# Performance work log

Measured on AMD Instinct MI355X. Metric: run time of the kernel, lower is better.

The kernel has to match this reference:

```python
import jax, jax.numpy as jnp
import numpy as np

COMMITMENT_W = 0.1
PROXIMITY_W = 0.33

def setup_inputs() -> dict:
    key = jax.random.key(0)
    k1, k2, k3 = jax.random.split(key, 3)
    N, B, C, H, W = 2, 16, 64, 64, 64
    P, D = 16, 64
    input_data = jax.random.normal(k1, (N, B, C, H, W), dtype=jnp.float32)
    codebook = jax.random.uniform(k2, (P, D), dtype=jnp.float32, minval=-1.0 / P, maxval=1.0 / P)
    previous_active_vectors = jax.random.uniform(k3, (P, D), dtype=jnp.float32, minval=-1.0 / P, maxval=1.0 / P)
    return {"input_data": input_data, "codebook": codebook,
            "previous_active_vectors": previous_active_vectors,
            "num_active_vectors": 16}


def reference(input_data, codebook, previous_active_vectors, num_active_vectors):
    # input_data: (N, B, C, H, W); codebook: (P, D) with D == C
    D = codebook.shape[1]
    N, B, C, H, W = input_data.shape
    # (N*B, H, W, C) channels-last, matching permute(0,2,3,1)
    x = input_data.reshape(N * B, C, H, W).transpose(0, 2, 3, 1)
    flat = x.reshape(-1, D)                              # (T, D)
    x2 = jnp.sum(flat * flat, axis=1, keepdims=True)     # (T, 1)

    n_levels = int(np.log2(num_active_vectors))
    quantized_list, losses = [], []
    for level in range(n_levels):
        nv = 2 ** (level + 1)
        active = codebook[:nv]                           # (nv, D)
        # squared euclidean distances (T, nv)
        dist = x2 + jnp.sum(active * active, axis=1) - 2.0 * (flat @ active.T)
        idx = jnp.argmin(dist, axis=1)                   # (T,)
        q = active[idx].reshape(x.shape)                 # (N*B, H, W, C); same as onehot @ active

        quant_loss = jnp.mean((q - jax.lax.stop_gradient(x)) ** 2)
        align_loss = jnp.mean((jax.lax.stop_gradient(q) - x) ** 2) if level in (0, 1) else 0.0
        prox_loss = (level * PROXIMITY_W *
                     jnp.mean((previous_active_vectors[:nv // 2] - active[:nv // 2]) ** 2)
                     ) if level >= 1 else 0.0
        losses.append(quant_loss + COMMITMENT_W * align_loss + prox_loss)

        # straight-through estimator
        q = x + jax.lax.stop_gradient(q - x)
        quantized_list.append(q.transpose(0, 3, 1, 2))   # (N*B, C, H, W)

    return (jnp.stack(quantized_list),                   # (L, N*B, C, H, W)
            jnp.stack(losses),                           # (L,)
            codebook[:num_active_vectors])               # final active vectors
```

## Files before the change

### kernel.cpp

```cpp
#include <hip/hip_runtime.h>


namespace {

constexpr int D     = 64;
constexpr int P     = 16;
constexpr int NLEV  = 4;
constexpr int BLOCK = 256;
constexpr int NPOS  = 32 * 4096;
constexpr int NBLK  = NPOS / BLOCK;

__global__ __launch_bounds__(BLOCK) void avq_main(
    const float* __restrict__ in,
    const float* __restrict__ cb,
    float* __restrict__ out,
    float* __restrict__ partial)
{
  __shared__ float cb_s[P][D + 1];
  __shared__ float cb2_s[P];
  __shared__ float wred[4 * NLEV];

  const int tid = threadIdx.x;
  for (int i = tid; i < P * D; i += BLOCK)
    cb_s[i >> 6][i & 63] = cb[i];
  __syncthreads();
  if (tid < P) {
    float s = 0.f;
    #pragma unroll
    for (int c = 0; c < D; ++c) { const float v = cb_s[tid][c]; s = fmaf(v, v, s); }
    cb2_s[tid] = s;
  }
  __syncthreads();

  const int p  = blockIdx.x * BLOCK + tid;
  const int n  = p >> 12;
  const int hw = p & 4095;
  const float* __restrict__ src = in + (n << 18) + hw;

  float dot[P];
  #pragma unroll
  for (int q = 0; q < P; ++q) dot[q] = 0.f;
  float x2 = 0.f;

  #pragma unroll
  for (int c = 0; c < D; ++c) {
    const float xv = src[c << 12];
    x2 = fmaf(xv, xv, x2);
    #pragma unroll
    for (int q = 0; q < P; ++q) dot[q] = fmaf(xv, cb_s[q][c], dot[q]);
  }

  float rel[P];
  #pragma unroll
  for (int q = 0; q < P; ++q) rel[q] = fmaf(-2.f, dot[q], cb2_s[q]);

  int   idx[NLEV];
  float err[NLEV];
  {
    int bi = 0; float bv = rel[0];
    if (rel[1] < bv) { bv = rel[1]; bi = 1; }
    idx[0] = bi; err[0] = x2 + bv;
    #pragma unroll
    for (int q = 2; q < 4; ++q)  if (rel[q] < bv) { bv = rel[q]; bi = q; }
    idx[1] = bi; err[1] = x2 + bv;
    #pragma unroll
    for (int q = 4; q < 8; ++q)  if (rel[q] < bv) { bv = rel[q]; bi = q; }
    idx[2] = bi; err[2] = x2 + bv;
    #pragma unroll
    for (int q = 8; q < 16; ++q) if (rel[q] < bv) { bv = rel[q]; bi = q; }
    idx[3] = bi; err[3] = x2 + bv;
  }

  float* __restrict__ dstbase = out + (n << 18) + hw;
  #pragma unroll
  for (int l = 0; l < NLEV; ++l) {
    const float* __restrict__ row = cb_s[idx[l]];
    float* __restrict__ dst = dstbase + (l << 23);
    #pragma unroll
    for (int c = 0; c < D; ++c) dst[c << 12] = row[c];
  }

  const int lane = tid & 63, wv = tid >> 6;
  #pragma unroll
  for (int l = 0; l < NLEV; ++l) {
    float v = err[l];
    #pragma unroll
    for (int off = 32; off > 0; off >>= 1) v += __shfl_down(v, off, 64);
    if (lane == 0) wred[wv * NLEV + l] = v;
  }
  __syncthreads();
  if (tid < NLEV) {
    partial[blockIdx.x * NLEV + tid] =
        wred[0 * NLEV + tid] + wred[1 * NLEV + tid] +
        wred[2 * NLEV + tid] + wred[3 * NLEV + tid];
  }
}

__device__ inline float block_sum256(float v, float* sbuf, int tid) {
  #pragma unroll
  for (int off = 32; off > 0; off >>= 1) v += __shfl_down(v, off, 64);
  __syncthreads();
  if ((tid & 63) == 0) sbuf[tid >> 6] = v;
  __syncthreads();
  const float r = sbuf[0] + sbuf[1] + sbuf[2] + sbuf[3];
  __syncthreads();
  return r;
}

__global__ __launch_bounds__(BLOCK) void avq_final(
    const float* __restrict__ partial,
    const float* __restrict__ cb,
    const float* __restrict__ prev,
    float* __restrict__ out)
{
  __shared__ float sbuf[4];
  const int tid = threadIdx.x;
  float* __restrict__ losses = out + (NLEV << 23);
  float* __restrict__ cbout  = losses + NLEV;

  for (int i = tid; i < P * D; i += BLOCK) cbout[i] = cb[i];

  float s0 = 0.f, s1 = 0.f, s2 = 0.f, s3 = 0.f;
  for (int b = tid; b < NBLK; b += BLOCK) {
    s0 += partial[b * NLEV + 0];
    s1 += partial[b * NLEV + 1];
    s2 += partial[b * NLEV + 2];
    s3 += partial[b * NLEV + 3];
  }

  float p1 = 0.f, p2 = 0.f, p3 = 0.f;
  for (int e = tid; e < 8 * D; e += BLOCK) {
    const float dlt = prev[e] - cb[e];
    const float d2  = dlt * dlt;
    const int   r   = e >> 6;
    if (r < 2) p1 += d2;
    if (r < 4) p2 += d2;
    p3 += d2;
  }

  s0 = block_sum256(s0, sbuf, tid);
  s1 = block_sum256(s1, sbuf, tid);
  s2 = block_sum256(s2, sbuf, tid);
  s3 = block_sum256(s3, sbuf, tid);
  p1 = block_sum256(p1, sbuf, tid);
  p2 = block_sum256(p2, sbuf, tid);
  p3 = block_sum256(p3, sbuf, tid);

  if (tid == 0) {
    const float inv = 1.0f / 8388608.0f;
    const float ql0 = s0 * inv, ql1 = s1 * inv, ql2 = s2 * inv, ql3 = s3 * inv;
    losses[0] = ql0 + 0.1f * ql0;
    losses[1] = ql1 + 0.1f * ql1 + 1.0f * 0.33f * (p1 * (1.0f / 128.0f));
    losses[2] = ql2 + 2.0f * 0.33f * (p2 * (1.0f / 256.0f));
    losses[3] = ql3 + 3.0f * 0.33f * (p3 * (1.0f / 512.0f));
  }
}

}

extern "C" void kernel_launch(void* const* d_in, const int* in_sizes, int n_in,
                              void* d_out, int out_size, void* d_ws, size_t ws_size,
                              hipStream_t stream) {
  const float* in   = (const float*)d_in[0];
  const float* cb   = (const float*)d_in[1];
  const float* prev = (const float*)d_in[2];
  float* out     = (float*)d_out;
  float* partial = (float*)d_ws;

  avq_main<<<NBLK, BLOCK, 0, stream>>>(in, cb, out, partial);
  avq_final<<<1, BLOCK, 0, stream>>>(partial, cb, prev, out);
}
```

Before: 42.69 us.

## Split quantization into index-assign and vectorized codebook-expand kernels

```diff
diff --git a/kernel.cpp b/kernel.cpp
--- a/kernel.cpp
+++ b/kernel.cpp
@@ -3,36 +3,43 @@
 
 namespace {
 
-constexpr int D     = 64;
-constexpr int P     = 16;
-constexpr int NLEV  = 4;
-constexpr int BLOCK = 256;
-constexpr int NPOS  = 32 * 4096;
-constexpr int NBLK  = NPOS / BLOCK;
+typedef float f32x4 __attribute__((ext_vector_type(4)));
 
-__global__ __launch_bounds__(BLOCK) void avq_main(
-    const float* __restrict__ in,
-    const float* __restrict__ cb,
-    float* __restrict__ out,
-    float* __restrict__ partial)
+constexpr int D      = 64;
+constexpr int P      = 16;
+constexpr int NLEV   = 4;
+constexpr int NPOS   = 32 * 4096;
+constexpr int ABLK   = 64;
+constexpr int NBLK_A = NPOS / ABLK;
+constexpr int BBLK   = 256;
+constexpr int QPT    = 4;
+constexpr int NQUAD  = NLEV * NPOS * (D / 4);
+constexpr int NBLK_B = NQUAD / (BBLK * QPT);
+
+__global__ __launch_bounds__(ABLK) void avq_assign(
+    const float* __restrict__ in, const float* __restrict__ cb,
+    float* __restrict__ partial, unsigned char* __restrict__ idx8)
 {
-  __shared__ float cb_s[P][D + 1];
+  __shared__ f32x4 cb4_s[P][D / 4];
   __shared__ float cb2_s[P];
-  __shared__ float wred[4 * NLEV];
 
   const int tid = threadIdx.x;
-  for (int i = tid; i < P * D; i += BLOCK)
-    cb_s[i >> 6][i & 63] = cb[i];
+  for (int i = tid; i < P * (D / 4); i += ABLK)
+    cb4_s[i >> 4][i & 15] = ((const f32x4*)cb)[i];
   __syncthreads();
   if (tid < P) {
     float s = 0.f;
     #pragma unroll
-    for (int c = 0; c < D; ++c) { const float v = cb_s[tid][c]; s = fmaf(v, v, s); }
+    for (int j = 0; j < D / 4; ++j) {
+      const f32x4 v = cb4_s[tid][j];
+      s = fmaf(v.x, v.x, s); s = fmaf(v.y, v.y, s);
+      s = fmaf(v.z, v.z, s); s = fmaf(v.w, v.w, s);
+    }
     cb2_s[tid] = s;
   }
   __syncthreads();
 
-  const int p  = blockIdx.x * BLOCK + tid;
+  const int p  = blockIdx.x * ABLK + tid;
   const int n  = p >> 12;
   const int hw = p & 4095;
   const float* __restrict__ src = in + (n << 18) + hw;
@@ -43,56 +50,49 @@
   float x2 = 0.f;
 
   #pragma unroll
-  for (int c = 0; c < D; ++c) {
-    const float xv = src[c << 12];
-    x2 = fmaf(xv, xv, x2);
+  for (int c4 = 0; c4 < D / 4; ++c4) {
+    const float xv0 = src[(c4 * 4 + 0) << 12];
+    const float xv1 = src[(c4 * 4 + 1) << 12];
+    const float xv2 = src[(c4 * 4 + 2) << 12];
+    const float xv3 = src[(c4 * 4 + 3) << 12];
+    x2 = fmaf(xv0, xv0, x2); x2 = fmaf(xv1, xv1, x2);
+    x2 = fmaf(xv2, xv2, x2); x2 = fmaf(xv3, xv3, x2);
     #pragma unroll
-    for (int q = 0; q < P; ++q) dot[q] = fmaf(xv, cb_s[q][c], dot[q]);
+    for (int q = 0; q < P; ++q) {
+      const f32x4 cv = cb4_s[q][c4];
+      float dq = dot[q];
+      dq = fmaf(xv0, cv.x, dq); dq = fmaf(xv1, cv.y, dq);
+      dq = fmaf(xv2, cv.z, dq); dq = fmaf(xv3, cv.w, dq);
+      dot[q] = dq;
+    }
   }
 
   float rel[P];
   #pragma unroll
   for (int q = 0; q < P; ++q) rel[q] = fmaf(-2.f, dot[q], cb2_s[q]);
 
-  int   idx[NLEV];
   float err[NLEV];
   {
     int bi = 0; float bv = rel[0];
     if (rel[1] < bv) { bv = rel[1]; bi = 1; }
-    idx[0] = bi; err[0] = x2 + bv;
+    idx8[0 * NPOS + p] = (unsigned char)bi; err[0] = x2 + bv;
     #pragma unroll
     for (int q = 2; q < 4; ++q)  if (rel[q] < bv) { bv = rel[q]; bi = q; }
-    idx[1] = bi; err[1] = x2 + bv;
+    idx8[1 * NPOS + p] = (unsigned char)bi; err[1] = x2 + bv;
     #pragma unroll
     for (int q = 4; q < 8; ++q)  if (rel[q] < bv) { bv = rel[q]; bi = q; }
-    idx[2] = bi; err[2] = x2 + bv;
+    idx8[2 * NPOS + p] = (unsigned char)bi; err[2] = x2 + bv;
     #pragma unroll
     for (int q = 8; q < 16; ++q) if (rel[q] < bv) { bv = rel[q]; bi = q; }
-    idx[3] = bi; err[3] = x2 + bv;
+    idx8[3 * NPOS + p] = (unsigned char)bi; err[3] = x2 + bv;
   }
 
-  float* __restrict__ dstbase = out + (n << 18) + hw;
-  #pragma unroll
-  for (int l = 0; l < NLEV; ++l) {
-    const float* __restrict__ row = cb_s[idx[l]];
-    float* __restrict__ dst = dstbase + (l << 23);
-    #pragma unroll
-    for (int c = 0; c < D; ++c) dst[c << 12] = row[c];
-  }
-
-  const int lane = tid & 63, wv = tid >> 6;
   #pragma unroll
   for (int l = 0; l < NLEV; ++l) {
     float v = err[l];
     #pragma unroll
     for (int off = 32; off > 0; off >>= 1) v += __shfl_down(v, off, 64);
-    if (lane == 0) wred[wv * NLEV + l] = v;
-  }
-  __syncthreads();
-  if (tid < NLEV) {
-    partial[blockIdx.x * NLEV + tid] =
-        wred[0 * NLEV + tid] + wred[1 * NLEV + tid] +
-        wred[2 * NLEV + tid] + wred[3 * NLEV + tid];
+    if (tid == 0) partial[blockIdx.x * NLEV + l] = v;
   }
 }
 
@@ -107,52 +107,74 @@
   return r;
 }
 
-__global__ __launch_bounds__(BLOCK) void avq_final(
-    const float* __restrict__ partial,
-    const float* __restrict__ cb,
-    const float* __restrict__ prev,
+__global__ __launch_bounds__(BBLK) void avq_expand(
+    const float* __restrict__ cb, const float* __restrict__ prev,
+    const float* __restrict__ partial, const unsigned char* __restrict__ idx8,
     float* __restrict__ out)
 {
+  __shared__ float col_s[P];
   __shared__ float sbuf[4];
   const int tid = threadIdx.x;
-  float* __restrict__ losses = out + (NLEV << 23);
-  float* __restrict__ cbout  = losses + NLEV;
 
-  for (int i = tid; i < P * D; i += BLOCK) cbout[i] = cb[i];
+  if (blockIdx.x == 0) {
+    float* __restrict__ losses = out + NQUAD * 4;
+    float* __restrict__ cbout  = losses + NLEV;
+    for (int i = tid; i < P * D; i += BBLK) cbout[i] = cb[i];
 
-  float s0 = 0.f, s1 = 0.f, s2 = 0.f, s3 = 0.f;
-  for (int b = tid; b < NBLK; b += BLOCK) {
-    s0 += partial[b * NLEV + 0];
-    s1 += partial[b * NLEV + 1];
-    s2 += partial[b * NLEV + 2];
-    s3 += partial[b * NLEV + 3];
+    float s0 = 0.f, s1 = 0.f, s2 = 0.f, s3 = 0.f;
+    for (int b = tid; b < NBLK_A; b += BBLK) {
+      s0 += partial[b * NLEV + 0];
+      s1 += partial[b * NLEV + 1];
+      s2 += partial[b * NLEV + 2];
+      s3 += partial[b * NLEV + 3];
+    }
+    float p1 = 0.f, p2 = 0.f, p3 = 0.f;
+    for (int e = tid; e < 8 * D; e += BBLK) {
+      const float dlt = prev[e] - cb[e];
+      const float d2  = dlt * dlt;
+      const int   r   = e >> 6;
+      if (r < 2) p1 += d2;
+      if (r < 4) p2 += d2;
+      p3 += d2;
+    }
+    s0 = block_sum256(s0, sbuf, tid);
+    s1 = block_sum256(s1, sbuf, tid);
+    s2 = block_sum256(s2, sbuf, tid);
+    s3 = block_sum256(s3, sbuf, tid);
+    p1 = block_sum256(p1, sbuf, tid);
+    p2 = block_sum256(p2, sbuf, tid);
+    p3 = block_sum256(p3, sbuf, tid);
+    if (tid == 0) {
+      const float inv = 1.0f / 8388608.0f;
+      const float ql0 = s0 * inv, ql1 = s1 * inv, ql2 = s2 * inv, ql3 = s3 * inv;
+      losses[0] = ql0 + 0.1f * ql0;
+      losses[1] = ql1 + 0.1f * ql1 + 1.0f * 0.33f * (p1 * (1.0f / 128.0f));
+      losses[2] = ql2 + 2.0f * 0.33f * (p2 * (1.0f / 256.0f));
+      losses[3] = ql3 + 3.0f * 0.33f * (p3 * (1.0f / 512.0f));
+    }
+    return;
   }
 
-  float p1 = 0.f, p2 = 0.f, p3 = 0.f;
-  for (int e = tid; e < 8 * D; e += BLOCK) {
-    const float dlt = prev[e] - cb[e];
-    const float d2  = dlt * dlt;
-    const int   r   = e >> 6;
-    if (r < 2) p1 += d2;
-    if (r < 4) p2 += d2;
-    p3 += d2;
-  }
+  const int b  = blockIdx.x - 1;
+  const int ln = b >> 6;
+  const int c  = b & 63;
 
-  s0 = block_sum256(s0, sbuf, tid);
-  s1 = block_sum256(s1, sbuf, tid);
-  s2 = block_sum256(s2, sbuf, tid);
-  s3 = block_sum256(s3, sbuf, tid);
-  p1 = block_sum256(p1, sbuf, tid);
-  p2 = block_sum256(p2, sbuf, tid);
-  p3 = block_sum256(p3, sbuf, tid);
+  if (tid < P) col_s[tid] = cb[tid * D + c];
+  __syncthreads();
 
-  if (tid == 0) {
-    const float inv = 1.0f / 8388608.0f;
-    const float ql0 = s0 * inv, ql1 = s1 * inv, ql2 = s2 * inv, ql3 = s3 * inv;
-    losses[0] = ql0 + 0.1f * ql0;
-    losses[1] = ql1 + 0.1f * ql1 + 1.0f * 0.33f * (p1 * (1.0f / 128.0f));
-    losses[2] = ql2 + 2.0f * 0.33f * (p2 * (1.0f / 256.0f));
-    losses[3] = ql3 + 3.0f * 0.33f * (p3 * (1.0f / 512.0f));
+  const unsigned* __restrict__ packs = (const unsigned*)idx8 + (ln << 10);
+  float* __restrict__ dst = out + ((long)b << 12);
+
+  #pragma unroll
+  for (int it = 0; it < QPT; ++it) {
+    const int hwq = (it << 8) + tid;
+    const unsigned pack = packs[hwq];
+    f32x4 v;
+    v.x = col_s[pack & 15];
+    v.y = col_s[(pack >> 8) & 15];
+    v.z = col_s[(pack >> 16) & 15];
+    v.w = col_s[(pack >> 24) & 15];
+    __builtin_nontemporal_store(v, (f32x4*)dst + hwq);
   }
 }
 
@@ -164,9 +186,11 @@
   const float* in   = (const float*)d_in[0];
   const float* cb   = (const float*)d_in[1];
   const float* prev = (const float*)d_in[2];
-  float* out     = (float*)d_out;
-  float* partial = (float*)d_ws;
+  float* out = (float*)d_out;
 
-  avq_main<<<NBLK, BLOCK, 0, stream>>>(in, cb, out, partial);
-  avq_final<<<1, BLOCK, 0, stream>>>(partial, cb, prev, out);
+  float* partial        = (float*)d_ws;
+  unsigned char* idx8   = (unsigned char*)d_ws + NBLK_A * NLEV * sizeof(float);
+
+  avq_assign<<<NBLK_A, ABLK, 0, stream>>>(in, cb, partial, idx8);
+  avq_expand<<<NBLK_B + 1, BBLK, 0, stream>>>(cb, prev, partial, idx8, out);
 }
```

Result: faster. 40.28 us (-5.6%).
